# Performance work log

Hardware: AMD Instinct MI355X
Metric: run time of the kernel (lower is better)

Reference implementation:

```python
import jax, jax.numpy as jnp
import numpy as np

N = 50000      # nodes
E = 800000     # edges (avg degree 16)
D_IN = 128     # node_feature_dim
H = 256        # hidden_dim
EPS = 1e-5     # BatchNorm eps


def setup_inputs() -> dict:
    key = jax.random.key(0)
    ks = jax.random.split(key, 32)
    inp = {
        "x": jax.random.normal(ks[0], (N, D_IN), jnp.float32),
        "edge_index": jax.random.randint(ks[1], (2, E), 0, N, jnp.int32),
    }
    dims = [(D_IN, H), (H, H), (H, H)]
    k = 2
    for i, (din, dout) in enumerate(dims):
        s = 1.0 / np.sqrt(din)
        inp[f"Wl{i}"] = jax.random.uniform(ks[k], (din, dout), jnp.float32, -s, s); k += 1
        inp[f"bl{i}"] = jax.random.uniform(ks[k], (dout,), jnp.float32, -s, s); k += 1
        inp[f"Wr{i}"] = jax.random.uniform(ks[k], (din, dout), jnp.float32, -s, s); k += 1
        inp[f"g{i}"] = jnp.ones((dout,), jnp.float32)
        inp[f"b{i}"] = jnp.zeros((dout,), jnp.float32)
        inp[f"rm{i}"] = jax.random.normal(ks[k], (dout,), jnp.float32) * 0.1; k += 1
        inp[f"rv{i}"] = jax.random.uniform(ks[k], (dout,), jnp.float32, 0.5, 1.5); k += 1
    return inp


def _sage(x, src, dst, Wl, bl, Wr):
    # PyG SAGEConv (aggr='mean'): out = lin_l(mean_{j in N(i)} x_j) + lin_r(x_i)
    deg = jax.ops.segment_sum(jnp.ones((src.shape[0],), x.dtype), dst, num_segments=N)
    agg = jax.ops.segment_sum(x[src], dst, num_segments=N)  # [N, d_in]
    mean = agg / jnp.maximum(deg, 1.0)[:, None]
    return mean @ Wl + bl + x @ Wr


def _bn(x, g, b, rm, rv):
    # eval-mode BatchNorm1d with running stats
    return (x - rm) * (g * jax.lax.rsqrt(rv + EPS)) + b


def reference(x, edge_index,
              Wl0, bl0, Wr0, g0, b0, rm0, rv0,
              Wl1, bl1, Wr1, g1, b1, rm1, rv1,
              Wl2, bl2, Wr2, g2, b2, rm2, rv2):
    src, dst = edge_index[0], edge_index[1]
    h = jax.nn.relu(_bn(_sage(x, src, dst, Wl0, bl0, Wr0), g0, b0, rm0, rv0))
    h = jax.nn.relu(_bn(_sage(h, src, dst, Wl1, bl1, Wr1), g1, b1, rm1, rv1))
    h = _bn(_sage(h, src, dst, Wl2, bl2, Wr2), g2, b2, rm2, rv2)
    return h  # [N, H] node embeddings (dropout is identity in eval mode)
```

## Files before the change

### kernel.cpp

```cpp
#include <hip/hip_runtime.h>
#include <hip/hip_bf16.h>

#define NNODES 50000
#define NEDGES 800000
#define HID 256
#define BN_EPS 1e-5f
#define SCAN_B ((NNODES + 255) / 256)

typedef __attribute__((ext_vector_type(8))) short short8v;
typedef __attribute__((ext_vector_type(4))) float f32x4;
typedef __attribute__((ext_vector_type(2))) float f32x2;

__device__ inline void load_lds16(const void* g, void* l) {
    __builtin_amdgcn_global_load_lds(
        (const __attribute__((address_space(1))) unsigned int*)g,
        (__attribute__((address_space(3))) unsigned int*)l, 16, 0, 0);
}

__global__ void k_countrank(const int* __restrict__ ei, int* __restrict__ cnt,
                            int* __restrict__ rank, int nE) {
    int e = blockIdx.x * blockDim.x + threadIdx.x;
    if (e < nE) rank[e] = atomicAdd(&cnt[ei[nE + e]], 1);
}

__global__ void k_bsum(const int* __restrict__ cnt, int* __restrict__ loc,
                       int* __restrict__ bsum, int n) {
    __shared__ int sh[256];
    int tid = threadIdx.x;
    int i = blockIdx.x * 256 + tid;
    int v = (i < n) ? cnt[i] : 0;
    sh[tid] = v;
    __syncthreads();
    for (int off = 1; off < 256; off <<= 1) {
        int t = (tid >= off) ? sh[tid - off] : 0;
        __syncthreads();
        sh[tid] += t;
        __syncthreads();
    }
    if (i < n) loc[i] = sh[tid] - v;
    if (tid == 255) bsum[blockIdx.x] = sh[255];
}

__global__ void k_bscan(int* __restrict__ bsum, int nb) {
    __shared__ int sh[256];
    int tid = threadIdx.x;
    int v = (tid < nb) ? bsum[tid] : 0;
    sh[tid] = v;
    __syncthreads();
    for (int off = 1; off < 256; off <<= 1) {
        int t = (tid >= off) ? sh[tid - off] : 0;
        __syncthreads();
        sh[tid] += t;
        __syncthreads();
    }
    if (tid < nb) bsum[tid] = sh[tid] - v;
}

__global__ void k_addoff(const int* __restrict__ loc, const int* __restrict__ bsum,
                         int* __restrict__ rowptr, int n, int nE) {
    int i = blockIdx.x * 256 + threadIdx.x;
    if (i < n) rowptr[i] = loc[i] + bsum[blockIdx.x];
    if (i == 0) rowptr[n] = nE;
}

__global__ void k_fill2(const int* __restrict__ ei, const int* __restrict__ rowptr,
                        const int* __restrict__ rank, int* __restrict__ col, int nE) {
    int e = blockIdx.x * blockDim.x + threadIdx.x;
    if (e < nE) col[rowptr[ei[nE + e]] + rank[e]] = ei[e];
}

#define PREP_CAST 1600000
#define PREP_TR   327680
__global__ void k_prep(const float* __restrict__ x,
                       __hip_bfloat16* __restrict__ xb, unsigned char* __restrict__ x8,
                       const float* __restrict__ s0, const float* __restrict__ s1,
                       const float* __restrict__ s2, const float* __restrict__ s3,
                       const float* __restrict__ s4, const float* __restrict__ s5,
                       __hip_bfloat16* __restrict__ d0, __hip_bfloat16* __restrict__ d1,
                       __hip_bfloat16* __restrict__ d2, __hip_bfloat16* __restrict__ d3,
                       __hip_bfloat16* __restrict__ d4, __hip_bfloat16* __restrict__ d5,
                       int* __restrict__ cnt) {
    int f = blockIdx.x * blockDim.x + threadIdx.x;
    if (f < PREP_CAST) {
        float4 v = *(const float4*)(x + f * 4);
        union { uint2 u; unsigned short s[4]; } ob;
        ob.s[0] = __bfloat16_as_ushort(__float2bfloat16(v.x));
        ob.s[1] = __bfloat16_as_ushort(__float2bfloat16(v.y));
        ob.s[2] = __bfloat16_as_ushort(__float2bfloat16(v.z));
        ob.s[3] = __bfloat16_as_ushort(__float2bfloat16(v.w));
        *(uint2*)(xb + f * 4) = ob.u;
        int p = __builtin_amdgcn_cvt_pk_fp8_f32(v.x, v.y, 0, false);
        p = __builtin_amdgcn_cvt_pk_fp8_f32(v.z, v.w, p, true);
        *(int*)(x8 + f * 4) = p;
    } else if (f < PREP_CAST + PREP_TR) {
        int r = f - PREP_CAST;
        const float* src; __hip_bfloat16* dst; int i;
        if (r < 65536) {
            if (r < 32768) { src = s0; dst = d0; i = r; }
            else           { src = s1; dst = d1; i = r - 32768; }
        } else {
            int q = r - 65536;
            int wsel = q >> 16;
            i = q & 65535;
            src = (wsel == 0) ? s2 : (wsel == 1) ? s3 : (wsel == 2) ? s4 : s5;
            dst = (wsel == 0) ? d2 : (wsel == 1) ? d3 : (wsel == 2) ? d4 : d5;
        }
        int k = i >> 8;
        int nn = i & 255;
        dst[((k >> 3) * 256 + nn) * 8 + (k & 7)] = __float2bfloat16(src[i]);
    } else {
        int i = f - PREP_CAST - PREP_TR;
        if (i < NNODES) cnt[i] = 0;
    }
}

template <int D, int U>
__global__ void k_meanf8(const unsigned char* __restrict__ x8,
                         const int* __restrict__ rowptr, const int* __restrict__ col,
                         __hip_bfloat16* __restrict__ mean, int n) {
    constexpr int CPL = D / 16;
    constexpr int R = 64 / CPL;
    int gw = (blockIdx.x * blockDim.x + threadIdx.x) >> 6;
    int lane = threadIdx.x & 63;
    if (gw >= n) return;
    int beg = rowptr[gw], end = rowptr[gw + 1];
    int sub = lane / CPL;
    int fpos = lane % CPL;
    const uint4* base = (const uint4*)x8;

    float acc[16];
#pragma unroll
    for (int j = 0; j < 16; j++) acc[j] = 0.f;

    for (int p0 = beg; p0 < end; p0 += U * R) {
        int idx[U]; bool ok[U];
#pragma unroll
        for (int u = 0; u < U; u++) {
            int p = p0 + u * R + sub;
            ok[u] = (p < end);
            idx[u] = ok[u] ? col[p] : 0;
        }
        uint4 v[U];
#pragma unroll
        for (int u = 0; u < U; u++) {
            uint4 t = {0u, 0u, 0u, 0u};
            if (ok[u]) t = base[(size_t)idx[u] * CPL + fpos];
            v[u] = t;
        }
#pragma unroll
        for (int u = 0; u < U; u++) {
            const unsigned int uu[4] = {v[u].x, v[u].y, v[u].z, v[u].w};
#pragma unroll
            for (int q = 0; q < 4; q++) {
                f32x2 lo = __builtin_amdgcn_cvt_pk_f32_fp8(uu[q], false);
                f32x2 hi = __builtin_amdgcn_cvt_pk_f32_fp8(uu[q], true);
                acc[4 * q + 0] += lo.x;
                acc[4 * q + 1] += lo.y;
                acc[4 * q + 2] += hi.x;
                acc[4 * q + 3] += hi.y;
            }
        }
    }

    if constexpr (R >= 8) {
#pragma unroll
        for (int j = 0; j < 16; j++) acc[j] += __shfl_xor(acc[j], 8, 64);
    }
#pragma unroll
    for (int j = 0; j < 16; j++) acc[j] += __shfl_xor(acc[j], 16, 64);
#pragma unroll
    for (int j = 0; j < 16; j++) acc[j] += __shfl_xor(acc[j], 32, 64);

    if (sub == 0) {
        float inv = (end > beg) ? 1.f / (float)(end - beg) : 0.f;
        union { uint4 v[2]; unsigned short s[16]; } o;
#pragma unroll
        for (int j = 0; j < 16; j++)
            o.s[j] = __bfloat16_as_ushort(__float2bfloat16(acc[j] * inv));
        uint4* dst = (uint4*)(mean + (size_t)gw * D + fpos * 16);
        dst[0] = o.v[0];
        dst[1] = o.v[1];
    }
}

template <int KH, typename OutT, int RELU, int W8>
__launch_bounds__(1024, 4)
__global__ void k_gemm6(const __hip_bfloat16* __restrict__ A1,
                        const __hip_bfloat16* __restrict__ A2,
                        const __hip_bfloat16* __restrict__ Wp,
                        const float* __restrict__ bl,
                        const float* __restrict__ g,
                        const float* __restrict__ bb,
                        const float* __restrict__ rm,
                        const float* __restrict__ rv,
                        OutT* __restrict__ out, unsigned char* __restrict__ out8,
                        int n) {
    constexpr int NSTEP = KH / 16;
    __shared__ char lds[65536];
    int tid = threadIdx.x;
    int rb = blockIdx.x;
    int lane = tid & 63, wv = tid >> 6;
    int quad = lane >> 4, ml = lane & 15;
    int wr = wv >> 2, wc = wv & 3;
    int row0 = rb * 128 + wr * 32;

    const short8v* p1[2];
    const short8v* p2[2];
#pragma unroll
    for (int i = 0; i < 2; i++) {
        int r = row0 + i * 16 + ml;
        if (r > n - 1) r = n - 1;
        p1[i] = (const short8v*)(A1 + (size_t)r * KH) + quad;
        p2[i] = (const short8v*)(A2 + (size_t)r * KH) + quad;
    }

    f32x4 acc[2][4];
#pragma unroll
    for (int i = 0; i < 2; i++)
#pragma unroll
        for (int t = 0; t < 4; t++) acc[i][t] = {0.f, 0.f, 0.f, 0.f};

    short8v ab[2][2];
    const char* wpb = (const char*)Wp;

    load_lds16(wpb + tid * 16, lds + tid * 16);
    ab[0][0] = p1[0][0];
    ab[0][1] = p1[1][0];
    __syncthreads();

#pragma unroll
    for (int s = 0; s < NSTEP; s++) {
        char* buf  = lds + (s & 1) * 16384;
        char* nbuf = lds + ((s + 1) & 1) * 16384;
        if (s + 1 < NSTEP) {
            load_lds16(wpb + (size_t)(s + 1) * 16384 + tid * 16, nbuf + tid * 16);
            int sn = s + 1;
            const short8v* const* pp = (sn < NSTEP / 2) ? p1 : p2;
            int sh = (sn < NSTEP / 2) ? sn : sn - NSTEP / 2;
            ab[sn & 1][0] = pp[0][sh * 4];
            ab[sn & 1][1] = pp[1][sh * 4];
        }
        short8v bfr[4];
#pragma unroll
        for (int t = 0; t < 4; t++)
            bfr[t] = *(const short8v*)(
                buf + (size_t)((quad * 256) + (wc * 64 + t * 16 + ml)) * 16);
#pragma unroll
        for (int t = 0; t < 4; t++) {
            acc[0][t] = __builtin_amdgcn_mfma_f32_16x16x32_bf16(
                ab[s & 1][0], bfr[t], acc[0][t], 0, 0, 0);
            acc[1][t] = __builtin_amdgcn_mfma_f32_16x16x32_bf16(
                ab[s & 1][1], bfr[t], acc[1][t], 0, 0, 0);
        }
        __syncthreads();
    }

    char* scrb = lds + wv * 4096;
    float sv[4], tv[4];
#pragma unroll
    for (int t = 0; t < 4; t++) {
        int c = wc * 64 + t * 16 + ml;
        sv[t] = g[c] * rsqrtf(rv[c] + BN_EPS);
        tv[t] = (bl[c] - rm[c]) * sv[t] + bb[c];
    }
    int rl8 = lane >> 3, c8 = (lane & 7) * 8;
#pragma unroll
    for (int p = 0; p < 2; p++) {
#pragma unroll
        for (int t = 0; t < 4; t++) {
#pragma unroll
            for (int r = 0; r < 4; r++) {
                float v = acc[p][t][r] * sv[t] + tv[t];
                if (RELU) v = fmaxf(v, 0.f);
                int rowl = quad * 4 + r;
                int off = rowl * 256 + (((t * 16 + ml) * 4) ^ ((rowl & 7) << 4));
                *(float*)(scrb + off) = v;
            }
        }
#pragma unroll
        for (int q = 0; q < 2; q++) {
            int rowl = q * 8 + rl8;
            int row = row0 + p * 16 + rowl;
            int sw = (rowl & 7) << 4;
            f32x4 v0 = *(const f32x4*)(scrb + rowl * 256 + ((c8 * 4) ^ sw));
            f32x4 v1 = *(const f32x4*)(scrb + rowl * 256 + ((c8 * 4 + 16) ^ sw));
            if (row < n) {
                int c0 = wc * 64 + c8;
                if constexpr (sizeof(OutT) == 2) {
                    union { uint4 u; unsigned short s[8]; } o;
                    o.s[0] = __bfloat16_as_ushort(__float2bfloat16(v0.x));
                    o.s[1] = __bfloat16_as_ushort(__float2bfloat16(v0.y));
                    o.s[2] = __bfloat16_as_ushort(__float2bfloat16(v0.z));
                    o.s[3] = __bfloat16_as_ushort(__float2bfloat16(v0.w));
                    o.s[4] = __bfloat16_as_ushort(__float2bfloat16(v1.x));
                    o.s[5] = __bfloat16_as_ushort(__float2bfloat16(v1.y));
                    o.s[6] = __bfloat16_as_ushort(__float2bfloat16(v1.z));
                    o.s[7] = __bfloat16_as_ushort(__float2bfloat16(v1.w));
                    *(uint4*)(out + (size_t)row * HID + c0) = o.u;
                } else {
                    float* dst = (float*)out + (size_t)row * HID + c0;
                    *(f32x4*)dst = v0;
                    *(f32x4*)(dst + 4) = v1;
                }
                if constexpr (W8) {
                    int lo = __builtin_amdgcn_cvt_pk_fp8_f32(v0.x, v0.y, 0, false);
                    lo = __builtin_amdgcn_cvt_pk_fp8_f32(v0.z, v0.w, lo, true);
                    int hi = __builtin_amdgcn_cvt_pk_fp8_f32(v1.x, v1.y, 0, false);
                    hi = __builtin_amdgcn_cvt_pk_fp8_f32(v1.z, v1.w, hi, true);
                    uint2 u2 = {(unsigned)lo, (unsigned)hi};
                    *(uint2*)(out8 + (size_t)row * HID + c0) = u2;
                }
            }
        }
    }
}

extern "C" void kernel_launch(void* const* d_in, const int* in_sizes, int n_in,
                              void* d_out, int out_size, void* d_ws, size_t ws_size,
                              hipStream_t stream) {
    const float* x = (const float*)d_in[0];
    const int* ei = (const int*)d_in[1];
    const float *Wl[3], *blv[3], *Wr[3], *g[3], *bb[3], *rm[3], *rv[3];
    for (int i = 0; i < 3; i++) {
        int b = 2 + i * 7;
        Wl[i]  = (const float*)d_in[b + 0];
        blv[i] = (const float*)d_in[b + 1];
        Wr[i]  = (const float*)d_in[b + 2];
        g[i]   = (const float*)d_in[b + 3];
        bb[i]  = (const float*)d_in[b + 4];
        rm[i]  = (const float*)d_in[b + 5];
        rv[i]  = (const float*)d_in[b + 6];
    }

    char* ob = (char*)d_out;
    __hip_bfloat16* xb = (__hip_bfloat16*)ob;
    __hip_bfloat16* h0 = (__hip_bfloat16*)(ob + (size_t)NNODES * 128 * 2);

    char* w = (char*)d_ws;
    size_t off = 0;
    auto alloc = [&](size_t bytes) {
        void* p = w + off;
        off += (bytes + 255) & ~(size_t)255;
        return p;
    };
    int* rowptr = (int*)alloc((NNODES + 1) * sizeof(int));
    int* cnt    = (int*)alloc(NNODES * sizeof(int));
    int* loc    = (int*)alloc(NNODES * sizeof(int));
    int* bsum   = (int*)alloc(SCAN_B * sizeof(int));
    int* rank   = (int*)alloc(NEDGES * sizeof(int));
    int* col    = (int*)alloc(NEDGES * sizeof(int));
    __hip_bfloat16* meanb = (__hip_bfloat16*)alloc((size_t)NNODES * HID * 2);
    __hip_bfloat16* h1    = (__hip_bfloat16*)alloc((size_t)NNODES * HID * 2);
    unsigned char* x8   = (unsigned char*)alloc((size_t)NNODES * 128);
    unsigned char* h0f8 = (unsigned char*)alloc((size_t)NNODES * HID);
    unsigned char* h1f8 = (unsigned char*)alloc((size_t)NNODES * HID);
    __hip_bfloat16* Wp0 = (__hip_bfloat16*)alloc((size_t)2 * 128 * 256 * 2);
    __hip_bfloat16* Wp1 = (__hip_bfloat16*)alloc((size_t)2 * 256 * 256 * 2);
    __hip_bfloat16* Wp2 = (__hip_bfloat16*)alloc((size_t)2 * 256 * 256 * 2);

    int prepTotal = PREP_CAST + PREP_TR + NNODES;
    k_prep<<<(prepTotal + 255) / 256, 256, 0, stream>>>(
        x, xb, x8, Wl[0], Wr[0], Wl[1], Wr[1], Wl[2], Wr[2],
        Wp0, Wp0 + 32768, Wp1, Wp1 + 65536, Wp2, Wp2 + 65536, cnt);

    k_countrank<<<(NEDGES + 255) / 256, 256, 0, stream>>>(ei, cnt, rank, NEDGES);
    k_bsum<<<SCAN_B, 256, 0, stream>>>(cnt, loc, bsum, NNODES);
    k_bscan<<<1, 256, 0, stream>>>(bsum, SCAN_B);
    k_addoff<<<SCAN_B, 256, 0, stream>>>(loc, bsum, rowptr, NNODES, NEDGES);
    k_fill2<<<(NEDGES + 255) / 256, 256, 0, stream>>>(ei, rowptr, rank, col, NEDGES);

    int meanBlocks = (NNODES * 64 + 255) / 256;
    int gemmBlocks = (NNODES + 127) / 128;

    k_meanf8<128, 2><<<meanBlocks, 256, 0, stream>>>(x8, rowptr, col, meanb, NNODES);
    k_gemm6<128, __hip_bfloat16, 1, 1><<<gemmBlocks, 1024, 0, stream>>>(meanb, xb, Wp0,
        blv[0], g[0], bb[0], rm[0], rv[0], h0, h0f8, NNODES);

    k_meanf8<256, 4><<<meanBlocks, 256, 0, stream>>>(h0f8, rowptr, col, meanb, NNODES);
    k_gemm6<256, __hip_bfloat16, 1, 1><<<gemmBlocks, 1024, 0, stream>>>(meanb, h0, Wp1,
        blv[1], g[1], bb[1], rm[1], rv[1], h1, h1f8, NNODES);

    k_meanf8<256, 4><<<meanBlocks, 256, 0, stream>>>(h1f8, rowptr, col, meanb, NNODES);
    k_gemm6<256, float, 0, 0><<<gemmBlocks, 1024, 0, stream>>>(meanb, h1, Wp2,
        blv[2], g[2], bb[2], rm[2], rv[2], (float*)d_out, (unsigned char*)nullptr, NNODES);
}
```

Baseline: 413.1 us.

## Fuse neighbor mean aggregation into GEMM kernel via LDS-staged A tile

Merges the fp8 gather-mean kernel into the SAGE GEMM. Each 1024-thread block first aggregates its 128 rows' neighbor means into a swizzled bf16 tile in LDS, then runs the MFMA loop reading the first half of K from LDS and the second half from global. This removes the bf16 mean buffer write and re-read plus one launch per layer. In exchange it raises LDS use (up to 96KB per block), which lowers occupancy, and it serializes the gather phase before the MFMA work within each block.

Result: slower. 430.2 us (+4.2%).

```diff
diff --git a/kernel.cpp b/kernel.cpp
--- a/kernel.cpp
+++ b/kernel.cpp
@@ -114,80 +114,12 @@
     }
 }
 
-template <int D, int U>
-__global__ void k_meanf8(const unsigned char* __restrict__ x8,
-                         const int* __restrict__ rowptr, const int* __restrict__ col,
-                         __hip_bfloat16* __restrict__ mean, int n) {
-    constexpr int CPL = D / 16;
-    constexpr int R = 64 / CPL;
-    int gw = (blockIdx.x * blockDim.x + threadIdx.x) >> 6;
-    int lane = threadIdx.x & 63;
-    if (gw >= n) return;
-    int beg = rowptr[gw], end = rowptr[gw + 1];
-    int sub = lane / CPL;
-    int fpos = lane % CPL;
-    const uint4* base = (const uint4*)x8;
-
-    float acc[16];
-#pragma unroll
-    for (int j = 0; j < 16; j++) acc[j] = 0.f;
-
-    for (int p0 = beg; p0 < end; p0 += U * R) {
-        int idx[U]; bool ok[U];
-#pragma unroll
-        for (int u = 0; u < U; u++) {
-            int p = p0 + u * R + sub;
-            ok[u] = (p < end);
-            idx[u] = ok[u] ? col[p] : 0;
-        }
-        uint4 v[U];
-#pragma unroll
-        for (int u = 0; u < U; u++) {
-            uint4 t = {0u, 0u, 0u, 0u};
-            if (ok[u]) t = base[(size_t)idx[u] * CPL + fpos];
-            v[u] = t;
-        }
-#pragma unroll
-        for (int u = 0; u < U; u++) {
-            const unsigned int uu[4] = {v[u].x, v[u].y, v[u].z, v[u].w};
-#pragma unroll
-            for (int q = 0; q < 4; q++) {
-                f32x2 lo = __builtin_amdgcn_cvt_pk_f32_fp8(uu[q], false);
-                f32x2 hi = __builtin_amdgcn_cvt_pk_f32_fp8(uu[q], true);
-                acc[4 * q + 0] += lo.x;
-                acc[4 * q + 1] += lo.y;
-                acc[4 * q + 2] += hi.x;
-                acc[4 * q + 3] += hi.y;
-            }
-        }
-    }
-
-    if constexpr (R >= 8) {
-#pragma unroll
-        for (int j = 0; j < 16; j++) acc[j] += __shfl_xor(acc[j], 8, 64);
-    }
-#pragma unroll
-    for (int j = 0; j < 16; j++) acc[j] += __shfl_xor(acc[j], 16, 64);
-#pragma unroll
-    for (int j = 0; j < 16; j++) acc[j] += __shfl_xor(acc[j], 32, 64);
-
-    if (sub == 0) {
-        float inv = (end > beg) ? 1.f / (float)(end - beg) : 0.f;
-        union { uint4 v[2]; unsigned short s[16]; } o;
-#pragma unroll
-        for (int j = 0; j < 16; j++)
-            o.s[j] = __bfloat16_as_ushort(__float2bfloat16(acc[j] * inv));
-        uint4* dst = (uint4*)(mean + (size_t)gw * D + fpos * 16);
-        dst[0] = o.v[0];
-        dst[1] = o.v[1];
-    }
-}
-
 template <int KH, typename OutT, int RELU, int W8>
 __launch_bounds__(1024, 4)
-__global__ void k_gemm6(const __hip_bfloat16* __restrict__ A1,
+__global__ void k_fused(const unsigned char* __restrict__ gtab,
                         const __hip_bfloat16* __restrict__ A2,
                         const __hip_bfloat16* __restrict__ Wp,
+                        const int* __restrict__ rowptr, const int* __restrict__ col,
                         const float* __restrict__ bl,
                         const float* __restrict__ g,
                         const float* __restrict__ bb,
@@ -196,21 +128,90 @@
                         OutT* __restrict__ out, unsigned char* __restrict__ out8,
                         int n) {
     constexpr int NSTEP = KH / 16;
-    __shared__ char lds[65536];
-    int tid = threadIdx.x;
-    int rb = blockIdx.x;
+    constexpr int NH = NSTEP / 2;
+    constexpr int ROWB = KH * 2;
+    constexpr int A1SZ = 128 * ROWB;
+    __shared__ char lds[A1SZ + 32768];
+    char* bbase = lds + A1SZ;
+    int tid = threadIdx.x, rb = blockIdx.x;
     int lane = tid & 63, wv = tid >> 6;
     int quad = lane >> 4, ml = lane & 15;
+
+    load_lds16((const char*)Wp + tid * 16, bbase + tid * 16);
+
+    {
+        constexpr int CPL = KH / 16;
+        constexpr int R = 64 / CPL;
+        constexpr int U = (KH == 128) ? 2 : 4;
+        int sub = lane / CPL, fpos = lane % CPL;
+        const uint4* base = (const uint4*)gtab;
+        for (int kk = 0; kk < 8; kk++) {
+            int rowl = wv * 8 + kk;
+            int nd = rb * 128 + rowl;
+            int beg = 0, end = 0;
+            if (nd < n) { beg = rowptr[nd]; end = rowptr[nd + 1]; }
+            float acc[16];
+#pragma unroll
+            for (int j = 0; j < 16; j++) acc[j] = 0.f;
+            for (int p0 = beg; p0 < end; p0 += U * R) {
+                int idx[U]; bool ok[U];
+#pragma unroll
+                for (int u = 0; u < U; u++) {
+                    int p = p0 + u * R + sub;
+                    ok[u] = (p < end);
+                    idx[u] = ok[u] ? col[p] : 0;
+                }
+                uint4 v[U];
+#pragma unroll
+                for (int u = 0; u < U; u++) {
+                    uint4 t = {0u, 0u, 0u, 0u};
+                    if (ok[u]) t = base[(size_t)idx[u] * CPL + fpos];
+                    v[u] = t;
+                }
+#pragma unroll
+                for (int u = 0; u < U; u++) {
+                    const unsigned int uu[4] = {v[u].x, v[u].y, v[u].z, v[u].w};
+#pragma unroll
+                    for (int q = 0; q < 4; q++) {
+                        f32x2 lo = __builtin_amdgcn_cvt_pk_f32_fp8(uu[q], false);
+                        f32x2 hi = __builtin_amdgcn_cvt_pk_f32_fp8(uu[q], true);
+                        acc[4 * q + 0] += lo.x;
+                        acc[4 * q + 1] += lo.y;
+                        acc[4 * q + 2] += hi.x;
+                        acc[4 * q + 3] += hi.y;
+                    }
+                }
+            }
+            if constexpr (R >= 8) {
+#pragma unroll
+                for (int j = 0; j < 16; j++) acc[j] += __shfl_xor(acc[j], 8, 64);
+            }
+#pragma unroll
+            for (int j = 0; j < 16; j++) acc[j] += __shfl_xor(acc[j], 16, 64);
+#pragma unroll
+            for (int j = 0; j < 16; j++) acc[j] += __shfl_xor(acc[j], 32, 64);
+            if (sub == 0) {
+                float inv = (end > beg) ? 1.f / (float)(end - beg) : 0.f;
+                union { uint4 v[2]; unsigned short s[16]; } o;
+#pragma unroll
+                for (int j = 0; j < 16; j++)
+                    o.s[j] = __bfloat16_as_ushort(__float2bfloat16(acc[j] * inv));
+                char* rp = lds + (size_t)rowl * ROWB;
+                *(uint4*)(rp + ((2 * fpos + 0) ^ (rowl & 15)) * 16) = o.v[0];
+                *(uint4*)(rp + ((2 * fpos + 1) ^ (rowl & 15)) * 16) = o.v[1];
+            }
+        }
+    }
+    __syncthreads();
+
     int wr = wv >> 2, wc = wv & 3;
     int row0 = rb * 128 + wr * 32;
 
-    const short8v* p1[2];
     const short8v* p2[2];
 #pragma unroll
     for (int i = 0; i < 2; i++) {
         int r = row0 + i * 16 + ml;
         if (r > n - 1) r = n - 1;
-        p1[i] = (const short8v*)(A1 + (size_t)r * KH) + quad;
         p2[i] = (const short8v*)(A2 + (size_t)r * KH) + quad;
     }
 
@@ -223,22 +224,28 @@
     short8v ab[2][2];
     const char* wpb = (const char*)Wp;
 
-    load_lds16(wpb + tid * 16, lds + tid * 16);
-    ab[0][0] = p1[0][0];
-    ab[0][1] = p1[1][0];
-    __syncthreads();
-
 #pragma unroll
     for (int s = 0; s < NSTEP; s++) {
-        char* buf  = lds + (s & 1) * 16384;
-        char* nbuf = lds + ((s + 1) & 1) * 16384;
+        char* buf  = bbase + (s & 1) * 16384;
+        char* nbuf = bbase + ((s + 1) & 1) * 16384;
         if (s + 1 < NSTEP) {
             load_lds16(wpb + (size_t)(s + 1) * 16384 + tid * 16, nbuf + tid * 16);
-            int sn = s + 1;
-            const short8v* const* pp = (sn < NSTEP / 2) ? p1 : p2;
-            int sh = (sn < NSTEP / 2) ? sn : sn - NSTEP / 2;
-            ab[sn & 1][0] = pp[0][sh * 4];
-            ab[sn & 1][1] = pp[1][sh * 4];
+            if (s + 1 >= NH) {
+                int sh = s + 1 - NH;
+                ab[(s + 1) & 1][0] = p2[0][sh * 4];
+                ab[(s + 1) & 1][1] = p2[1][sh * 4];
+            }
+        }
+        short8v af0, af1;
+        if (s < NH) {
+            int c = s * 4 + quad;
+            int r0l = wr * 32 + ml;
+            int r1l = wr * 32 + 16 + ml;
+            af0 = *(const short8v*)(lds + (size_t)r0l * ROWB + ((c ^ (r0l & 15)) * 16));
+            af1 = *(const short8v*)(lds + (size_t)r1l * ROWB + ((c ^ (r1l & 15)) * 16));
+        } else {
+            af0 = ab[s & 1][0];
+            af1 = ab[s & 1][1];
         }
         short8v bfr[4];
 #pragma unroll
@@ -247,10 +254,8 @@
                 buf + (size_t)((quad * 256) + (wc * 64 + t * 16 + ml)) * 16);
 #pragma unroll
         for (int t = 0; t < 4; t++) {
-            acc[0][t] = __builtin_amdgcn_mfma_f32_16x16x32_bf16(
-                ab[s & 1][0], bfr[t], acc[0][t], 0, 0, 0);
-            acc[1][t] = __builtin_amdgcn_mfma_f32_16x16x32_bf16(
-                ab[s & 1][1], bfr[t], acc[1][t], 0, 0, 0);
+            acc[0][t] = __builtin_amdgcn_mfma_f32_16x16x32_bf16(af0, bfr[t], acc[0][t], 0, 0, 0);
+            acc[1][t] = __builtin_amdgcn_mfma_f32_16x16x32_bf16(af1, bfr[t], acc[1][t], 0, 0, 0);
         }
         __syncthreads();
     }
@@ -349,8 +354,7 @@
     int* bsum   = (int*)alloc(SCAN_B * sizeof(int));
     int* rank   = (int*)alloc(NEDGES * sizeof(int));
     int* col    = (int*)alloc(NEDGES * sizeof(int));
-    __hip_bfloat16* meanb = (__hip_bfloat16*)alloc((size_t)NNODES * HID * 2);
-    __hip_bfloat16* h1    = (__hip_bfloat16*)alloc((size_t)NNODES * HID * 2);
+    __hip_bfloat16* h1 = (__hip_bfloat16*)alloc((size_t)NNODES * HID * 2);
     unsigned char* x8   = (unsigned char*)alloc((size_t)NNODES * 128);
     unsigned char* h0f8 = (unsigned char*)alloc((size_t)NNODES * HID);
     unsigned char* h1f8 = (unsigned char*)alloc((size_t)NNODES * HID);
@@ -369,18 +373,17 @@
     k_addoff<<<SCAN_B, 256, 0, stream>>>(loc, bsum, rowptr, NNODES, NEDGES);
     k_fill2<<<(NEDGES + 255) / 256, 256, 0, stream>>>(ei, rowptr, rank, col, NEDGES);
 
-    int meanBlocks = (NNODES * 64 + 255) / 256;
-    int gemmBlocks = (NNODES + 127) / 128;
-
-    k_meanf8<128, 2><<<meanBlocks, 256, 0, stream>>>(x8, rowptr, col, meanb, NNODES);
-    k_gemm6<128, __hip_bfloat16, 1, 1><<<gemmBlocks, 1024, 0, stream>>>(meanb, xb, Wp0,
+    int fusedBlocks = (NNODES + 127) / 128;
+
+    k_fused<128, __hip_bfloat16, 1, 1><<<fusedBlocks, 1024, 0, stream>>>(
+        x8, xb, Wp0, rowptr, col,
         blv[0], g[0], bb[0], rm[0], rv[0], h0, h0f8, NNODES);
 
-    k_meanf8<256, 4><<<meanBlocks, 256, 0, stream>>>(h0f8, rowptr, col, meanb, NNODES);
-    k_gemm6<256, __hip_bfloat16, 1, 1><<<gemmBlocks, 1024, 0, stream>>>(meanb, h0, Wp1,
+    k_fused<256, __hip_bfloat16, 1, 1><<<fusedBlocks, 1024, 0, stream>>>(
+        h0f8, h0, Wp1, rowptr, col,
         blv[1], g[1], bb[1], rm[1], rv[1], h1, h1f8, NNODES);
 
-    k_meanf8<256, 4><<<meanBlocks, 256, 0, stream>>>(h1f8, rowptr, col, meanb, NNODES);
-    k_gemm6<256, float, 0, 0><<<gemmBlocks, 1024, 0, stream>>>(meanb, h1, Wp2,
+    k_fused<256, float, 0, 0><<<fusedBlocks, 1024, 0, stream>>>(
+        h1f8, h1, Wp2, rowptr, col,
         blv[2], g[2], bb[2], rm[2], rv[2], (float*)d_out, (unsigned char*)nullptr, NNODES);
 }
```

## Stage activation tiles in swizzled LDS and stream weights through registers

Applied to the files above, without the earlier changes.

The GEMM kernel now loads the whole 128-row activation tile for both inputs into LDS up front with an XOR swizzle, and prefetches weight fragments directly from global memory into registers each K-step instead of double-buffering weights through LDS. This removes the per-step __syncthreads and the LDS round-trip for weights, and gives coalesced bulk loads for activations. The cost is more LDS per block for KH=256, which could lower occupancy, plus redundant weight reads across waves that rely on cache hits.

Result: faster. 380.5 us (-7.9%).

```diff
diff --git a/kernel.cpp b/kernel.cpp
--- a/kernel.cpp
+++ b/kernel.cpp
@@ -185,7 +185,7 @@
 
 template <int KH, typename OutT, int RELU, int W8>
 __launch_bounds__(1024, 4)
-__global__ void k_gemm6(const __hip_bfloat16* __restrict__ A1,
+__global__ void k_gemm7(const __hip_bfloat16* __restrict__ A1,
                         const __hip_bfloat16* __restrict__ A2,
                         const __hip_bfloat16* __restrict__ Wp,
                         const float* __restrict__ bl,
@@ -196,65 +196,70 @@
                         OutT* __restrict__ out, unsigned char* __restrict__ out8,
                         int n) {
     constexpr int NSTEP = KH / 16;
-    __shared__ char lds[65536];
-    int tid = threadIdx.x;
-    int rb = blockIdx.x;
+    constexpr int NH = NSTEP / 2;
+    constexpr int CH = KH / 8;
+    constexpr int ROWB = KH * 2;
+    constexpr int ASZ = 128 * ROWB;
+    __shared__ char lds[2 * ASZ];
+    int tid = threadIdx.x, rb = blockIdx.x;
     int lane = tid & 63, wv = tid >> 6;
     int quad = lane >> 4, ml = lane & 15;
+
+#pragma unroll
+    for (int it = 0; it < CH / 8; it++) {
+        int j = tid + it * 1024;
+        int r = j / CH, c = j % CH;
+        int grow = rb * 128 + r; if (grow > n - 1) grow = n - 1;
+        int cs = c ^ (r & 15);
+        load_lds16(A1 + (size_t)grow * KH + cs * 8, lds + (size_t)j * 16);
+        load_lds16(A2 + (size_t)grow * KH + cs * 8, lds + ASZ + (size_t)j * 16);
+    }
+
     int wr = wv >> 2, wc = wv & 3;
     int row0 = rb * 128 + wr * 32;
 
-    const short8v* p1[2];
-    const short8v* p2[2];
-#pragma unroll
-    for (int i = 0; i < 2; i++) {
-        int r = row0 + i * 16 + ml;
-        if (r > n - 1) r = n - 1;
-        p1[i] = (const short8v*)(A1 + (size_t)r * KH) + quad;
-        p2[i] = (const short8v*)(A2 + (size_t)r * KH) + quad;
-    }
-
     f32x4 acc[2][4];
 #pragma unroll
     for (int i = 0; i < 2; i++)
 #pragma unroll
         for (int t = 0; t < 4; t++) acc[i][t] = {0.f, 0.f, 0.f, 0.f};
 
-    short8v ab[2][2];
-    const char* wpb = (const char*)Wp;
-
-    load_lds16(wpb + tid * 16, lds + tid * 16);
-    ab[0][0] = p1[0][0];
-    ab[0][1] = p1[1][0];
+    const uint4* wq = (const uint4*)Wp;
+    int bch = quad * 256 + wc * 64 + ml;
+    uint4 bpre[4];
+#pragma unroll
+    for (int t = 0; t < 4; t++) bpre[t] = wq[bch + t * 16];
+
     __syncthreads();
 
 #pragma unroll
     for (int s = 0; s < NSTEP; s++) {
-        char* buf  = lds + (s & 1) * 16384;
-        char* nbuf = lds + ((s + 1) & 1) * 16384;
+        uint4 bcur[4];
+#pragma unroll
+        for (int t = 0; t < 4; t++) bcur[t] = bpre[t];
         if (s + 1 < NSTEP) {
-            load_lds16(wpb + (size_t)(s + 1) * 16384 + tid * 16, nbuf + tid * 16);
-            int sn = s + 1;
-            const short8v* const* pp = (sn < NSTEP / 2) ? p1 : p2;
-            int sh = (sn < NSTEP / 2) ? sn : sn - NSTEP / 2;
-            ab[sn & 1][0] = pp[0][sh * 4];
-            ab[sn & 1][1] = pp[1][sh * 4];
-        }
-        short8v bfr[4];
-#pragma unroll
-        for (int t = 0; t < 4; t++)
-            bfr[t] = *(const short8v*)(
-                buf + (size_t)((quad * 256) + (wc * 64 + t * 16 + ml)) * 16);
+#pragma unroll
+            for (int t = 0; t < 4; t++)
+                bpre[t] = wq[(size_t)(s + 1) * 1024 + bch + t * 16];
+        }
+        const char* areg = (s < NH) ? lds : lds + ASZ;
+        int sl = (s < NH) ? s : s - NH;
+        short8v af[2];
+#pragma unroll
+        for (int i = 0; i < 2; i++) {
+            int r = wr * 32 + i * 16 + ml;
+            int c = sl * 4 + quad;
+            af[i] = *(const short8v*)(areg + (size_t)r * ROWB + ((c ^ (r & 15)) << 4));
+        }
 #pragma unroll
         for (int t = 0; t < 4; t++) {
-            acc[0][t] = __builtin_amdgcn_mfma_f32_16x16x32_bf16(
-                ab[s & 1][0], bfr[t], acc[0][t], 0, 0, 0);
-            acc[1][t] = __builtin_amdgcn_mfma_f32_16x16x32_bf16(
-                ab[s & 1][1], bfr[t], acc[1][t], 0, 0, 0);
-        }
-        __syncthreads();
-    }
-
+            short8v bf = *(const short8v*)&bcur[t];
+            acc[0][t] = __builtin_amdgcn_mfma_f32_16x16x32_bf16(af[0], bf, acc[0][t], 0, 0, 0);
+            acc[1][t] = __builtin_amdgcn_mfma_f32_16x16x32_bf16(af[1], bf, acc[1][t], 0, 0, 0);
+        }
+    }
+
+    __syncthreads();
     char* scrb = lds + wv * 4096;
     float sv[4], tv[4];
 #pragma unroll
@@ -373,14 +378,14 @@
     int gemmBlocks = (NNODES + 127) / 128;
 
     k_meanf8<128, 2><<<meanBlocks, 256, 0, stream>>>(x8, rowptr, col, meanb, NNODES);
-    k_gemm6<128, __hip_bfloat16, 1, 1><<<gemmBlocks, 1024, 0, stream>>>(meanb, xb, Wp0,
+    k_gemm7<128, __hip_bfloat16, 1, 1><<<gemmBlocks, 1024, 0, stream>>>(meanb, xb, Wp0,
         blv[0], g[0], bb[0], rm[0], rv[0], h0, h0f8, NNODES);
 
     k_meanf8<256, 4><<<meanBlocks, 256, 0, stream>>>(h0f8, rowptr, col, meanb, NNODES);
-    k_gemm6<256, __hip_bfloat16, 1, 1><<<gemmBlocks, 1024, 0, stream>>>(meanb, h0, Wp1,
+    k_gemm7<256, __hip_bfloat16, 1, 1><<<gemmBlocks, 1024, 0, stream>>>(meanb, h0, Wp1,
         blv[1], g[1], bb[1], rm[1], rv[1], h1, h1f8, NNODES);
 
-    k_meanf8<256, 4><<<meanBlocks, 256, 0, stream>>>(h1f8, rowptr, col, meanb, NNODES);
-    k_gemm6<256, float, 0, 0><<<gemmBlocks, 1024, 0, stream>>>(meanb, h1, Wp2,
+    k_meanf8<256, 4><<<gemmBlocks * 0 + meanBlocks, 256, 0, stream>>>(h1f8, rowptr, col, meanb, NNODES);
+    k_gemm7<256, float, 0, 0><<<gemmBlocks, 1024, 0, stream>>>(meanb, h1, Wp2,
         blv[2], g[2], bb[2], rm[2], rv[2], (float*)d_out, (unsigned char*)nullptr, NNODES);
 }
```
